# Kernel optimization log

Measured on AMD Instinct MI355X. Metric: run time of the kernel, lower is better.

## Reference

```python
import jax, jax.numpy as jnp
import numpy as np

B, S, E, H = 4, 2048, 1024, 16
K = 9           # number of boundaries per batch (K-1 = 8 passages)
DH = E // H


def make_relevance_mask(boundaries, relevance_scores, seq_len):
    """Vectorized equivalent of the Python-loop mask builder.

    boundaries: (B, K) int, sorted; boundaries[:,0] == q_end.
    relevance_scores: (B, K-1) float.
    Returns float mask (B, S, S) with values {0, 1, relevance}.
    """
    Bsz, Kb = boundaries.shape
    idx = jnp.arange(seq_len, dtype=boundaries.dtype)
    # pid[b, s] = j s.t. boundaries[b, j] <= s < boundaries[b, j+1]; -1 before b[0]
    pid = jax.vmap(lambda bb: jnp.searchsorted(bb, idx, side='right'))(boundaries) - 1  # (B,S)
    in_pass = (pid >= 0) & (pid < Kb - 1)  # inside some passage span
    rel_g = jnp.take_along_axis(relevance_scores, jnp.clip(pid, 0, Kb - 2), axis=1)  # (B,S)
    # query rows (pos < q_end): columns in passage j -> relevance[j], else 1
    col_val = jnp.where(in_pass, rel_g, 1.0)  # (B,S)
    qrow = idx[None, :] < boundaries[:, :1]   # (B,S)
    # non-query rows: 1 iff same passage block, else 0
    same = in_pass[:, :, None] & in_pass[:, None, :] & (pid[:, :, None] == pid[:, None, :])
    mask = jnp.where(qrow[:, :, None], col_val[:, None, :], jnp.where(same, 1.0, 0.0))
    return mask.astype(jnp.float32)


def setup_inputs() -> dict:
    key = jax.random.key(0)
    k1, k2, k3, k4, k5, k6, k7 = jax.random.split(key, 7)
    hidden_states = jax.random.normal(k1, (B, S, E), dtype=jnp.float32)
    relevance_scores = jax.random.uniform(k2, (B, K - 1), dtype=jnp.float32)
    passage_boundaries = jnp.sort(jax.random.randint(k3, (B, K), 0, S, dtype=jnp.int32), axis=1)
    in_proj_w = 0.02 * jax.random.normal(k4, (3 * E, E), dtype=jnp.float32)
    in_proj_b = jnp.zeros((3 * E,), dtype=jnp.float32)
    out_w = 0.02 * jax.random.normal(k5, (E, E), dtype=jnp.float32)
    out_b = jnp.zeros((E,), dtype=jnp.float32)
    return {
        'hidden_states': hidden_states,
        'relevance_scores': relevance_scores,
        'passage_boundaries': passage_boundaries,
        'in_proj_w': in_proj_w,
        'in_proj_b': in_proj_b,
        'out_w': out_w,
        'out_b': out_b,
    }


def reference(hidden_states, relevance_scores, passage_boundaries,
              in_proj_w, in_proj_b, out_w, out_b):
    Bsz, Sl, Em = hidden_states.shape
    mask = make_relevance_mask(passage_boundaries, relevance_scores, Sl)  # (B,S,S)
    qkv = hidden_states @ in_proj_w.T + in_proj_b              # (B,S,3E)
    q, k, v = jnp.split(qkv, 3, axis=-1)
    def heads(t):
        return t.reshape(Bsz, Sl, H, DH).transpose(0, 2, 1, 3)  # (B,H,S,Dh)
    q, k, v = heads(q), heads(k), heads(v)
    scale = 1.0 / jnp.sqrt(jnp.float32(DH))
    scores = jnp.einsum('bhqd,bhkd->bhqk', q * scale, k) + mask[:, None]  # float mask is ADDED
    attn = jax.nn.softmax(scores, axis=-1)
    out = jnp.einsum('bhqk,bhkd->bhqd', attn, v)
    out = out.transpose(0, 2, 1, 3).reshape(Bsz, Sl, Em)
    return out @ out_w.T + out_b
```

## Files before the change

### kernel.cpp

```cpp
#include <hip/hip_runtime.h>
#include <math.h>

#define Bsz 4
#define Sq  2048
#define Eq  1024
#define Hh  16
#define DHd 64
#define Kb  9
#define LOG2E 1.44269504088896340736f
#define NCLS 10

typedef _Float16 f16;
typedef __attribute__((ext_vector_type(8))) _Float16 fh8;
typedef __attribute__((ext_vector_type(4))) _Float16 fh4;
typedef __attribute__((ext_vector_type(2))) _Float16 fh2;
typedef __attribute__((ext_vector_type(4))) float fx4;
typedef __attribute__((ext_vector_type(16))) float fx16;
typedef __attribute__((ext_vector_type(4))) int i4;

#define SWZ(r, c) ((r) * 64 + ((c) ^ (((r) & 7) << 3)))

static __device__ __forceinline__ float fexp2(float x) {
#if __has_builtin(__builtin_amdgcn_exp2f)
  return __builtin_amdgcn_exp2f(x);
#else
  return __expf(x * 0.6931471805599453f);
#endif
}

__global__ void pid_kernel(const int* __restrict__ bnd, const float* __restrict__ rel,
                           int* __restrict__ pidr, float* __restrict__ lfTab) {
  int idx = blockIdx.x * blockDim.x + threadIdx.x;
  if (idx >= Bsz * Sq) return;
  int b = idx >> 11;
  int s = idx & (Sq - 1);
  int j = -1;
#pragma unroll
  for (int t = 0; t < Kb; ++t) {
    if (bnd[b * Kb + t] <= s) j = t;
  }
  pidr[idx] = j;
  bool inp = (j >= 0 && j < Kb - 1);
  float cv = inp ? rel[b * (Kb - 1) + j] : 1.0f;
  float* base = &lfTab[(size_t)b * NCLS * Sq + s];
  base[0] = cv * LOG2E;
#pragma unroll
  for (int c = 1; c < NCLS; ++c)
    base[c * Sq] = (inp && j == c - 1) ? LOG2E : 0.0f;
}

__global__ __launch_bounds__(256) void cvt_hs(const float* __restrict__ x,
                                              f16* __restrict__ xo) {
  int i = (blockIdx.x * blockDim.x + threadIdx.x) * 8;
  float4 a = *(const float4*)&x[i];
  float4 b = *(const float4*)&x[i + 4];
  fh8 o;
  o[0] = (f16)a.x; o[1] = (f16)a.y; o[2] = (f16)a.z; o[3] = (f16)a.w;
  o[4] = (f16)b.x; o[5] = (f16)b.y; o[6] = (f16)b.z; o[7] = (f16)b.w;
  *(fh8*)&xo[i] = o;
}

template <int MODE>
__global__ __launch_bounds__(256) void gemm_f16(
    const f16* __restrict__ A, const f16* __restrict__ Bh,
    const float* __restrict__ bias, float* __restrict__ Cp,
    int M, int N, int Kd,
    f16* __restrict__ qo, f16* __restrict__ ko, f16* __restrict__ vto) {
  __shared__ __align__(16) f16 Ash[128 * 64];
  __shared__ __align__(16) f16 Bsh[128 * 64];

  const int tid = threadIdx.x;
  const int lane = tid & 63, w = tid >> 6;
  const int wm = w >> 1, wn = w & 1;
  const int q16 = lane & 15, quad = lane >> 4;
  const int m_blk = blockIdx.y * 128, n_blk = blockIdx.x * 128;

  fx4 acc[4][4];
#pragma unroll
  for (int mt = 0; mt < 4; ++mt)
#pragma unroll
    for (int nt = 0; nt < 4; ++nt)
#pragma unroll
      for (int r = 0; r < 4; ++r) acc[mt][nt][r] = 0.f;

  const int sr = tid >> 2, sc = (tid & 3) * 16;

  fh8 pa[2][2], pb[2][2];
  const f16* ga0 = &A[(size_t)(m_blk + sr) * Kd + sc];
  const f16* gb0 = &Bh[(size_t)(n_blk + sr) * Kd + sc];

#pragma unroll
  for (int h = 0; h < 2; ++h) {
    const f16* ga = ga0 + (size_t)h * 64 * Kd;
    pa[h][0] = *(const fh8*)&ga[0];
    pa[h][1] = *(const fh8*)&ga[8];
    const f16* gb = gb0 + (size_t)h * 64 * Kd;
    pb[h][0] = *(const fh8*)&gb[0];
    pb[h][1] = *(const fh8*)&gb[8];
  }

  for (int k0 = 0; k0 < Kd; k0 += 64) {
    __syncthreads();
#pragma unroll
    for (int h = 0; h < 2; ++h) {
      const int r = sr + h * 64;
      *(fh8*)&Ash[SWZ(r, sc)]     = pa[h][0];
      *(fh8*)&Ash[SWZ(r, sc + 8)] = pa[h][1];
      *(fh8*)&Bsh[SWZ(r, sc)]     = pb[h][0];
      *(fh8*)&Bsh[SWZ(r, sc + 8)] = pb[h][1];
    }
    if (k0 + 64 < Kd) {
      const int kn = k0 + 64;
#pragma unroll
      for (int h = 0; h < 2; ++h) {
        const f16* ga = ga0 + (size_t)h * 64 * Kd + kn;
        pa[h][0] = *(const fh8*)&ga[0];
        pa[h][1] = *(const fh8*)&ga[8];
        const f16* gb = gb0 + (size_t)h * 64 * Kd + kn;
        pb[h][0] = *(const fh8*)&gb[0];
        pb[h][1] = *(const fh8*)&gb[8];
      }
    }
    __syncthreads();

#pragma unroll
    for (int ks = 0; ks < 2; ++ks) {
      fh8 af[4], bfr[4];
#pragma unroll
      for (int mt = 0; mt < 4; ++mt)
        af[mt] = *(const fh8*)&Ash[SWZ(wm * 64 + mt * 16 + q16, ks * 32 + quad * 8)];
#pragma unroll
      for (int nt = 0; nt < 4; ++nt)
        bfr[nt] = *(const fh8*)&Bsh[SWZ(wn * 64 + nt * 16 + q16, ks * 32 + quad * 8)];
#pragma unroll
      for (int nt = 0; nt < 4; ++nt)
#pragma unroll
        for (int mt = 0; mt < 4; ++mt)
          acc[mt][nt] = __builtin_amdgcn_mfma_f32_16x16x32_f16(af[mt], bfr[nt], acc[mt][nt], 0, 0, 0);
    }
  }

  float bsv[4];
#pragma unroll
  for (int nt = 0; nt < 4; ++nt) bsv[nt] = bias[n_blk + wn * 64 + nt * 16 + q16];

  if (MODE == 0) {
#pragma unroll
    for (int mt = 0; mt < 4; ++mt)
#pragma unroll
      for (int r = 0; r < 4; ++r) {
        int row = m_blk + wm * 64 + mt * 16 + quad * 4 + r;
#pragma unroll
        for (int nt = 0; nt < 4; ++nt) {
          int col = n_blk + wn * 64 + nt * 16 + q16;
          Cp[(size_t)row * N + col] = acc[mt][nt][r] + bsv[nt];
        }
      }
  } else {
    const int n0 = n_blk + wn * 64;
    const int which = n0 >> 10;
    const int hd = (n0 & 1023) >> 6;
    const float scale = (which == 0) ? 0.125f * LOG2E : 1.0f;
#pragma unroll
    for (int mt = 0; mt < 4; ++mt)
#pragma unroll
      for (int r = 0; r < 4; ++r) {
        int m = m_blk + wm * 64 + mt * 16 + quad * 4 + r;
        int b = m >> 11, s = m & (Sq - 1);
#pragma unroll
        for (int nt = 0; nt < 4; ++nt) {
          int d = nt * 16 + q16;
          float x = (acc[mt][nt][r] + bsv[nt]) * scale;
          if (which == 2) {
            vto[(((size_t)(b * Hh + hd)) * DHd + d) * Sq + s] = (f16)x;
          } else {
            f16* dst = (which == 0) ? qo : ko;
            dst[(((size_t)(b * Hh + hd)) * Sq + s) * DHd + d] = (f16)x;
          }
        }
      }
  }
}

__global__ __launch_bounds__(256, 2) void attn_v6(
    const f16* __restrict__ Qf, const f16* __restrict__ Kf,
    const f16* __restrict__ Vt, const int* __restrict__ pidr,
    const float* __restrict__ lfTab, f16* __restrict__ attf) {
  const int lin = blockIdx.x;
  const int orig = (lin & 7) * 128 + (lin >> 3);
  const int qb = orig & 15, hd = (orig >> 4) & 15, b = orig >> 8;
  const int bh = b * Hh + hd;
  const int tid = threadIdx.x;
  const int lane = tid & 63, w = tid >> 6;
  const int l31 = lane & 31, hi = lane >> 5;

  __shared__ __align__(16) f16 Ks[2][64 * 64];
  __shared__ __align__(16) f16 Vs[2][64 * 64];

  const size_t qkbase = (size_t)bh * Sq * DHd;
  const size_t vtbase = (size_t)bh * DHd * Sq;
  const int qrow = qb * 128 + w * 32 + l31;

  fh8 qf[4];
  {
    const f16* qp = &Qf[qkbase + (size_t)qrow * DHd + hi * 8];
#pragma unroll
    for (int ds = 0; ds < 4; ++ds) qf[ds] = *(const fh8*)&qp[ds * 16];
  }

  const int rq = pidr[b * Sq + qrow];
  const float* lfrow = &lfTab[((size_t)(b * NCLS + (rq + 1))) * Sq + 4 * hi];

  fh8 onesf;
#pragma unroll
  for (int j = 0; j < 8; ++j) onesf[j] = (l31 == 0) ? (f16)1.0f : (f16)0.0f;

  fx16 o_acc[2], lacc;
#pragma unroll
  for (int r = 0; r < 16; ++r) { o_acc[0][r] = 0.f; o_acc[1][r] = 0.f; lacc[r] = 0.f; }

  const int sr = tid >> 2, sc = (tid & 3) * 16;
  const int NT = Sq / 64;

  fh8 kc0, kc1, vc0, vc1;
  {
    const f16* gk = &Kf[qkbase + (size_t)sr * DHd + sc];
    kc0 = *(const fh8*)&gk[0]; kc1 = *(const fh8*)&gk[8];
    const f16* gv = &Vt[vtbase + (size_t)sr * Sq + sc];
    vc0 = *(const fh8*)&gv[0]; vc1 = *(const fh8*)&gv[8];
  }
  *(fh8*)&Ks[0][SWZ(sr, sc)]     = kc0;
  *(fh8*)&Ks[0][SWZ(sr, sc + 8)] = kc1;
  *(fh8*)&Vs[0][SWZ(sr, sc)]     = vc0;
  *(fh8*)&Vs[0][SWZ(sr, sc + 8)] = vc1;
  {
    const f16* gk = &Kf[qkbase + (size_t)(64 + sr) * DHd + sc];
    kc0 = *(const fh8*)&gk[0]; kc1 = *(const fh8*)&gk[8];
    const f16* gv = &Vt[vtbase + (size_t)sr * Sq + 64 + sc];
    vc0 = *(const fh8*)&gv[0]; vc1 = *(const fh8*)&gv[8];
  }
  __syncthreads();

  fx16 sacc0, sacc1;

  for (int kt = 0; kt < NT; ++kt) {
    const int c = kt & 1;

    {
      const float* lp = &lfrow[kt * 64];
#pragma unroll
      for (int g = 0; g < 4; ++g) {
        float4 a = *(const float4*)&lp[8 * g];
        sacc0[4 * g + 0] = a.x; sacc0[4 * g + 1] = a.y;
        sacc0[4 * g + 2] = a.z; sacc0[4 * g + 3] = a.w;
      }
    }

    if (kt + 1 < NT) {
      *(fh8*)&Ks[c ^ 1][SWZ(sr, sc)]     = kc0;
      *(fh8*)&Ks[c ^ 1][SWZ(sr, sc + 8)] = kc1;
      *(fh8*)&Vs[c ^ 1][SWZ(sr, sc)]     = vc0;
      *(fh8*)&Vs[c ^ 1][SWZ(sr, sc + 8)] = vc1;
      if (kt + 2 < NT) {
        const f16* gk = &Kf[qkbase + (size_t)((kt + 2) * 64 + sr) * DHd + sc];
        kc0 = *(const fh8*)&gk[0]; kc1 = *(const fh8*)&gk[8];
        const f16* gv = &Vt[vtbase + (size_t)sr * Sq + (kt + 2) * 64 + sc];
        vc0 = *(const fh8*)&gv[0]; vc1 = *(const fh8*)&gv[8];
      }
    }

    auto half = [&](fx16& sacc, int s, bool preload_next) {
      fh8 kfr[4];
#pragma unroll
      for (int ds = 0; ds < 4; ++ds)
        kfr[ds] = *(const fh8*)&Ks[c][SWZ(s * 32 + l31, ds * 16 + hi * 8)];
      __builtin_amdgcn_s_setprio(1);
#pragma unroll
      for (int ds = 0; ds < 4; ++ds)
        sacc = __builtin_amdgcn_mfma_f32_32x32x16_f16(kfr[ds], qf[ds], sacc, 0, 0, 0);
      __builtin_amdgcn_s_setprio(0);

      if (preload_next) {
        const float* lp = &lfrow[kt * 64 + 32];
#pragma unroll
        for (int g = 0; g < 4; ++g) {
          float4 a = *(const float4*)&lp[8 * g];
          sacc1[4 * g + 0] = a.x; sacc1[4 * g + 1] = a.y;
          sacc1[4 * g + 2] = a.z; sacc1[4 * g + 3] = a.w;
        }
      }

      int pk[8];
#pragma unroll
      for (int i = 0; i < 8; ++i) {
        fh2 h;
        h[0] = (f16)fexp2(sacc[2 * i]);
        h[1] = (f16)fexp2(sacc[2 * i + 1]);
        pk[i] = __builtin_bit_cast(int, h);
      }

      fh8 vfr[2][2];
#pragma unroll
      for (int dt = 0; dt < 2; ++dt)
#pragma unroll
        for (int kb = 0; kb < 2; ++kb)
          vfr[dt][kb] = *(const fh8*)&Vs[c][SWZ(dt * 32 + l31, s * 32 + kb * 16 + hi * 8)];

      __builtin_amdgcn_s_setprio(1);
#pragma unroll
      for (int kb = 0; kb < 2; ++kb) {
        int a01 = pk[4 * kb + 0], a23 = pk[4 * kb + 1];
        int a45 = pk[4 * kb + 2], a67 = pk[4 * kb + 3];
        i4 t;
#if __has_builtin(__builtin_amdgcn_permlane32_swap)
        auto s0 = __builtin_amdgcn_permlane32_swap(a01, a45, false, false);
        auto s1 = __builtin_amdgcn_permlane32_swap(a23, a67, false, false);
        t[0] = s0[0]; t[1] = s1[0]; t[2] = s0[1]; t[3] = s1[1];
#else
        int x01 = __shfl_xor(a01, 32), x23 = __shfl_xor(a23, 32);
        int x45 = __shfl_xor(a45, 32), x67 = __shfl_xor(a67, 32);
        t[0] = hi ? x45 : a01; t[1] = hi ? x67 : a23;
        t[2] = hi ? a45 : x01; t[3] = hi ? a67 : x23;
#endif
        fh8 pf = __builtin_bit_cast(fh8, t);
        lacc = __builtin_amdgcn_mfma_f32_32x32x16_f16(onesf, pf, lacc, 0, 0, 0);
        o_acc[0] = __builtin_amdgcn_mfma_f32_32x32x16_f16(vfr[0][kb], pf, o_acc[0], 0, 0, 0);
        o_acc[1] = __builtin_amdgcn_mfma_f32_32x32x16_f16(vfr[1][kb], pf, o_acc[1], 0, 0, 0);
      }
      __builtin_amdgcn_s_setprio(0);
    };

    half(sacc0, 0, true);
    half(sacc1, 1, false);

    if (kt + 1 < NT) __syncthreads();
  }

  float l = __shfl(lacc[0], l31);
  float inv = 1.0f / l;
  size_t obase = ((size_t)(b * Sq + qrow)) * Eq + hd * 64 + 4 * hi;
#pragma unroll
  for (int dt = 0; dt < 2; ++dt)
#pragma unroll
    for (int g = 0; g < 4; ++g) {
      fh4 o4;
#pragma unroll
      for (int j = 0; j < 4; ++j) o4[j] = (f16)(o_acc[dt][4 * g + j] * inv);
      *(fh4*)&attf[obase + dt * 32 + 8 * g] = o4;
    }
}

extern "C" void kernel_launch(void* const* d_in, const int* in_sizes, int n_in,
                              void* d_out, int out_size, void* d_ws, size_t ws_size,
                              hipStream_t stream) {
  const float* hs = (const float*)d_in[0];
  const float* rel = (const float*)d_in[1];
  const int* bnd = (const int*)d_in[2];
  const float* wi = (const float*)d_in[3];
  const float* bi = (const float*)d_in[4];
  const float* wo = (const float*)d_in[5];
  const float* bo = (const float*)d_in[6];
  float* out = (float*)d_out;

  const size_t NQ = (size_t)Bsz * Hh * Sq * DHd;
  char* p = (char*)d_ws;
  f16* qf = (f16*)p;   p += NQ * 2;
  f16* kf = (f16*)p;   p += NQ * 2;
  f16* vt = (f16*)p;   p += NQ * 2;
  f16* hsf = (f16*)p;  p += NQ * 2;
  f16* attf = (f16*)p; p += NQ * 2;
  f16* wif = (f16*)p;  p += (size_t)3 * Eq * Eq * 2;
  f16* wof = (f16*)p;  p += (size_t)Eq * Eq * 2;
  int* pidr = (int*)p; p += Bsz * Sq * 4;
  float* lfTab = (float*)p;

  hipLaunchKernelGGL(pid_kernel, dim3((Bsz * Sq + 255) / 256), dim3(256), 0, stream,
                     bnd, rel, pidr, lfTab);
  hipLaunchKernelGGL(cvt_hs, dim3((int)(NQ / 2048)), dim3(256), 0, stream, hs, hsf);
  hipLaunchKernelGGL(cvt_hs, dim3(3 * Eq * Eq / 2048), dim3(256), 0, stream, wi, wif);
  hipLaunchKernelGGL(cvt_hs, dim3(Eq * Eq / 2048), dim3(256), 0, stream, wo, wof);
  hipLaunchKernelGGL((gemm_f16<1>), dim3(24, 64), dim3(256), 0, stream,
                     hsf, wif, bi, (float*)nullptr, Bsz * Sq, 3 * Eq, Eq,
                     qf, kf, vt);
  hipLaunchKernelGGL(attn_v6, dim3(16 * 16 * 4), dim3(256), 0, stream,
                     qf, kf, vt, pidr, lfTab, attf);
  hipLaunchKernelGGL((gemm_f16<0>), dim3(8, 64), dim3(256), 0, stream,
                     attf, wof, bo, out, Bsz * Sq, Eq, Eq,
                     nullptr, nullptr, nullptr);
}
```

Measured before the change: 301.8 us.

## Double-buffer GEMM LDS tiles with direct global-to-LDS async loads

```diff
diff --git a/kernel.cpp b/kernel.cpp
--- a/kernel.cpp
+++ b/kernel.cpp
@@ -66,8 +66,8 @@
     const float* __restrict__ bias, float* __restrict__ Cp,
     int M, int N, int Kd,
     f16* __restrict__ qo, f16* __restrict__ ko, f16* __restrict__ vto) {
-  __shared__ __align__(16) f16 Ash[128 * 64];
-  __shared__ __align__(16) f16 Bsh[128 * 64];
+  __shared__ __align__(16) f16 Ash[2][128 * 64];
+  __shared__ __align__(16) f16 Bsh[2][128 * 64];
 
   const int tid = threadIdx.x;
   const int lane = tid & 63, w = tid >> 6;
@@ -83,61 +83,54 @@
 #pragma unroll
       for (int r = 0; r < 4; ++r) acc[mt][nt][r] = 0.f;
 
-  const int sr = tid >> 2, sc = (tid & 3) * 16;
-
-  fh8 pa[2][2], pb[2][2];
-  const f16* ga0 = &A[(size_t)(m_blk + sr) * Kd + sc];
-  const f16* gb0 = &Bh[(size_t)(n_blk + sr) * Kd + sc];
-
-#pragma unroll
-  for (int h = 0; h < 2; ++h) {
-    const f16* ga = ga0 + (size_t)h * 64 * Kd;
-    pa[h][0] = *(const fh8*)&ga[0];
-    pa[h][1] = *(const fh8*)&ga[8];
-    const f16* gb = gb0 + (size_t)h * 64 * Kd;
-    pb[h][0] = *(const fh8*)&gb[0];
-    pb[h][1] = *(const fh8*)&gb[8];
-  }
+  const int rl = lane >> 3;
+  const int bc = ((lane & 7) * 8) ^ (rl << 3);
+  const f16* gA = A + (size_t)m_blk * Kd;
+  const f16* gB = Bh + (size_t)n_blk * Kd;
+
+  auto stage = [&](f16* dstA, f16* dstB, int k0) {
+#pragma unroll
+    for (int j = 0; j < 4; ++j) {
+      const int r = w * 32 + j * 8;
+      const f16* pa = gA + (size_t)(r + rl) * Kd + k0 + bc;
+      const f16* pb = gB + (size_t)(r + rl) * Kd + k0 + bc;
+#if __has_builtin(__builtin_amdgcn_global_load_lds)
+      __builtin_amdgcn_global_load_lds(
+          (const __attribute__((address_space(1))) void*)pa,
+          (__attribute__((address_space(3))) void*)(dstA + r * 64), 16, 0, 0);
+      __builtin_amdgcn_global_load_lds(
+          (const __attribute__((address_space(1))) void*)pb,
+          (__attribute__((address_space(3))) void*)(dstB + r * 64), 16, 0, 0);
+#else
+      *(fh8*)&dstA[r * 64 + lane * 8] = *(const fh8*)pa;
+      *(fh8*)&dstB[r * 64 + lane * 8] = *(const fh8*)pb;
+#endif
+    }
+  };
+
+  stage(Ash[0], Bsh[0], 0);
+  __syncthreads();
 
   for (int k0 = 0; k0 < Kd; k0 += 64) {
-    __syncthreads();
-#pragma unroll
-    for (int h = 0; h < 2; ++h) {
-      const int r = sr + h * 64;
-      *(fh8*)&Ash[SWZ(r, sc)]     = pa[h][0];
-      *(fh8*)&Ash[SWZ(r, sc + 8)] = pa[h][1];
-      *(fh8*)&Bsh[SWZ(r, sc)]     = pb[h][0];
-      *(fh8*)&Bsh[SWZ(r, sc + 8)] = pb[h][1];
-    }
-    if (k0 + 64 < Kd) {
-      const int kn = k0 + 64;
-#pragma unroll
-      for (int h = 0; h < 2; ++h) {
-        const f16* ga = ga0 + (size_t)h * 64 * Kd + kn;
-        pa[h][0] = *(const fh8*)&ga[0];
-        pa[h][1] = *(const fh8*)&ga[8];
-        const f16* gb = gb0 + (size_t)h * 64 * Kd + kn;
-        pb[h][0] = *(const fh8*)&gb[0];
-        pb[h][1] = *(const fh8*)&gb[8];
-      }
-    }
-    __syncthreads();
+    const int c = (k0 >> 6) & 1;
+    if (k0 + 64 < Kd) stage(Ash[c ^ 1], Bsh[c ^ 1], k0 + 64);
 
 #pragma unroll
     for (int ks = 0; ks < 2; ++ks) {
       fh8 af[4], bfr[4];
 #pragma unroll
       for (int mt = 0; mt < 4; ++mt)
-        af[mt] = *(const fh8*)&Ash[SWZ(wm * 64 + mt * 16 + q16, ks * 32 + quad * 8)];
+        af[mt] = *(const fh8*)&Ash[c][SWZ(wm * 64 + mt * 16 + q16, ks * 32 + quad * 8)];
 #pragma unroll
       for (int nt = 0; nt < 4; ++nt)
-        bfr[nt] = *(const fh8*)&Bsh[SWZ(wn * 64 + nt * 16 + q16, ks * 32 + quad * 8)];
+        bfr[nt] = *(const fh8*)&Bsh[c][SWZ(wn * 64 + nt * 16 + q16, ks * 32 + quad * 8)];
 #pragma unroll
       for (int nt = 0; nt < 4; ++nt)
 #pragma unroll
         for (int mt = 0; mt < 4; ++mt)
           acc[mt][nt] = __builtin_amdgcn_mfma_f32_16x16x32_f16(af[mt], bfr[nt], acc[mt][nt], 0, 0, 0);
     }
+    __syncthreads();
   }
 
   float bsv[4];
```

Measured after the change: 313.7 us. 1.04x slower.
